# Optimization experiments

Hardware: AMD Instinct MI355X
Metric: run time of the kernel (lower is better)

## Reference

```python
import jax, jax.numpy as jnp
import numpy as np

B, S, D, H, F, NL, V = 4, 2048, 512, 8, 2048, 4, 32000
DH = D // H
EPS = 1e-6
LN_EPS = 1e-5


def _xavier(k, shape):
    lim = (6.0 / (shape[-2] + shape[-1])) ** 0.5
    return jax.random.uniform(k, shape, jnp.float32, -lim, lim)


def setup_inputs() -> dict:
    key = jax.random.key(0)
    ks = jax.random.split(key, 12)
    x = jax.random.randint(ks[0], (B, S), 0, V)
    emb = jax.random.normal(ks[1], (V, D), jnp.float32) * 0.02
    # sinusoidal positional encoding
    pos = np.arange(S, dtype=np.float32)[:, None]
    div = np.exp(np.arange(0, D, 2, dtype=np.float32) * (-np.log(10000.0) / D))
    pe_np = np.zeros((S, D), np.float32)
    pe_np[:, 0::2] = np.sin(pos * div)
    pe_np[:, 1::2] = np.cos(pos * div)
    pe = jnp.asarray(pe_np)
    return {
        "x": x, "emb": emb, "pe": pe,
        "Wq": _xavier(ks[2], (NL, D, D)), "bq": jnp.zeros((NL, D)),
        "Wk": _xavier(ks[3], (NL, D, D)), "bk": jnp.zeros((NL, D)),
        "Wv": _xavier(ks[4], (NL, D, D)), "bv": jnp.zeros((NL, D)),
        "Wo": _xavier(ks[5], (NL, D, D)), "bo": jnp.zeros((NL, D)),
        "W1": _xavier(ks[6], (NL, D, F)), "b1": jnp.zeros((NL, F)),
        "W2": _xavier(ks[7], (NL, F, D)), "b2": jnp.zeros((NL, D)),
        "g1": jnp.ones((NL, D)), "be1": jnp.zeros((NL, D)),
        "g2": jnp.ones((NL, D)), "be2": jnp.zeros((NL, D)),
        "gf": jnp.ones((D,)), "bf": jnp.zeros((D,)),
    }


def _layer_norm(h, g, b):
    mu = jnp.mean(h, axis=-1, keepdims=True)
    var = jnp.mean((h - mu) ** 2, axis=-1, keepdims=True)
    return (h - mu) * jax.lax.rsqrt(var + LN_EPS) * g + b


def _phi(u):
    # elu(x) + 1 feature map of fast-transformers causal-linear attention
    return jax.nn.elu(u) + 1.0


def _causal_linear_attention(q, k, v, key_mask):
    # q, k, v: [B, S, H, DH]; key_mask: [B, S] (1 for valid keys)
    Q = _phi(q)
    K = _phi(k) * key_mask[:, :, None, None]
    # cumulative state sum_{j<=i} K_j outer V_j : [B, S, H, DH, DH]
    St = jnp.cumsum(K[..., :, None] * v[..., None, :], axis=1)
    num = jnp.einsum("bshd,bshde->bshe", Q, St)
    Z = 1.0 / (jnp.einsum("bshd,bshd->bsh", Q, jnp.cumsum(K, axis=1)) + EPS)
    return num * Z[..., None]


def reference(x, emb, pe, Wq, bq, Wk, bk, Wv, bv, Wo, bo,
              W1, b1, W2, b2, g1, be1, g2, be2, gf, bf):
    # length mask from nonzero token count (LengthMask semantics)
    lengths = jnp.sum(jnp.abs(x) != 0, axis=-1)  # [B]
    key_mask = (jnp.arange(S)[None, :] < lengths[:, None]).astype(jnp.float32)
    h = emb[x] + pe[None, :, :]  # [B, S, D]
    for i in range(NL):
        q = (h @ Wq[i] + bq[i]).reshape(B, S, H, DH)
        k = (h @ Wk[i] + bk[i]).reshape(B, S, H, DH)
        v = (h @ Wv[i] + bv[i]).reshape(B, S, H, DH)
        a = _causal_linear_attention(q, k, v, key_mask).reshape(B, S, D)
        a = a @ Wo[i] + bo[i]
        h = _layer_norm(h + a, g1[i], be1[i])
        y = jax.nn.relu(h @ W1[i] + b1[i]) @ W2[i] + b2[i]
        h = _layer_norm(h + y, g2[i], be2[i])
    return _layer_norm(h, gf, bf)
```

## Files before the change

### kernel.cpp

```cpp
#include <hip/hip_runtime.h>
#include <math.h>

#define NLAYER 4
#define BB 4
#define SS 2048
#define DD 512
#define HH 8
#define DH 64
#define FF 2048
#define TT (BB*SS)
#define LCH 64
#define NCH (SS/LCH)
#define LN_EPS 1e-5f
#define ATT_EPS 1e-6f

typedef __bf16 bf16x8 __attribute__((ext_vector_type(8)));
typedef float  f32x4  __attribute__((ext_vector_type(4)));
typedef float  f32x16 __attribute__((ext_vector_type(16)));

__device__ __forceinline__ unsigned short f2bf(float f) {
    union { float f; unsigned u; } a; a.f = f;
    unsigned u = a.u;
    unsigned r = (u + 0x7FFFu + ((u >> 16) & 1u)) >> 16;
    return (unsigned short)r;
}
__device__ __forceinline__ float bf2f(unsigned short s) {
    union { unsigned u; float f; } a; a.u = ((unsigned)s) << 16;
    return a.f;
}
__device__ __forceinline__ float phi_f(float u) {
    return u > 0.f ? u + 1.f : __expf(u);
}

__global__ __launch_bounds__(64)
void len_kernel(const int* __restrict__ x, int* __restrict__ len) {
    const int b = blockIdx.x;
    int cnt = 0;
    for (int s = threadIdx.x; s < SS; s += 64) cnt += (x[b * SS + s] != 0);
    #pragma unroll
    for (int off = 32; off; off >>= 1) cnt += __shfl_xor(cnt, off);
    if (threadIdx.x == 0) len[b] = cnt;
}

__global__ __launch_bounds__(256)
void embed_kernel(const int* __restrict__ x, const float* __restrict__ emb,
                  const float* __restrict__ pe, unsigned short* __restrict__ h) {
    int t = blockIdx.x * 256 + threadIdx.x;
    int row = t >> 6, q = t & 63;
    int tok = x[row];
    int s = row & (SS - 1);
    const float4* ep = (const float4*)(emb + (size_t)tok * DD);
    const float4* pp = (const float4*)(pe + (size_t)s * DD);
    float4 e0 = ep[q * 2], e1 = ep[q * 2 + 1];
    float4 p0 = pp[q * 2], p1 = pp[q * 2 + 1];
    ushort4 u0 = make_ushort4(f2bf(e0.x + p0.x), f2bf(e0.y + p0.y),
                              f2bf(e0.z + p0.z), f2bf(e0.w + p0.w));
    ushort4 u1 = make_ushort4(f2bf(e1.x + p1.x), f2bf(e1.y + p1.y),
                              f2bf(e1.z + p1.z), f2bf(e1.w + p1.w));
    size_t base = (size_t)row * DD + q * 8;
    *(ushort4*)(h + base) = u0;
    *(ushort4*)(h + base + 4) = u1;
}

__global__ __launch_bounds__(256)
void transpose_cvt(const float* __restrict__ src, unsigned short* __restrict__ dst,
                   int R, int C, size_t srcLS, size_t dstLS) {
    __shared__ float tile[32][33];
    const int z = blockIdx.z;
    src += (size_t)z * srcLS;
    dst += (size_t)z * dstLS;
    const int c0 = blockIdx.x * 32, r0 = blockIdx.y * 32;
    const int tx = threadIdx.x & 31, ty = threadIdx.x >> 5;
    #pragma unroll
    for (int i = 0; i < 32; i += 8)
        tile[ty + i][tx] = src[(size_t)(r0 + ty + i) * C + c0 + tx];
    __syncthreads();
    #pragma unroll
    for (int i = 0; i < 32; i += 8)
        dst[(size_t)(c0 + ty + i) * R + r0 + tx] = f2bf(tile[tx][ty + i]);
}

__global__ __launch_bounds__(256)
void bias_concat(const float* __restrict__ bq, const float* __restrict__ bk,
                 const float* __restrict__ bv, float* __restrict__ bqkv) {
    int idx = blockIdx.x * 256 + threadIdx.x;
    if (idx >= NLAYER * 1536) return;
    int l = idx / 1536, n = idx % 1536;
    float v = n < 512 ? bq[l * 512 + n] : (n < 1024 ? bk[l * 512 + n - 512] : bv[l * 512 + n - 1024]);
    bqkv[idx] = v;
}

__device__ __forceinline__ void gll16(void* lds_ptr, const void* g_ptr) {
    __builtin_amdgcn_global_load_lds(
        (const __attribute__((address_space(1))) void*)g_ptr,
        (__attribute__((address_space(3))) void*)lds_ptr, 16, 0, 0);
}

template<int RELU, int WB>
__global__ __launch_bounds__(256, 2)
void gemm_bt(const unsigned short* __restrict__ A, const unsigned short* __restrict__ Bt,
             const float* __restrict__ bias, float* __restrict__ Cf,
             unsigned short* __restrict__ Cb, int M, int N, int K) {
    __shared__ __align__(16) char lds[2 * 2 * 128 * 64 * 2];
    const int Nt = N >> 7;
    const int bid = blockIdx.x;
    const int swz = (bid & 7) * ((int)gridDim.x >> 3) + (bid >> 3);
    const int m0 = (swz / Nt) * 128;
    const int n0 = (swz % Nt) * 128;
    const int tid = threadIdx.x;
    const int w = tid >> 6, lane = tid & 63;
    const int wr = w >> 1, wc = w & 1;
    const int srow = lane >> 3, scc = lane & 7;
    const int l32 = lane & 31, khalf = lane >> 5;

    f32x16 acc[2][2] = {};

    auto stage = [&](int buf, int k0) {
        char* base = lds + buf * 32768;
        #pragma unroll
        for (int op = 0; op < 2; ++op) {
            const unsigned short* G = op ? Bt : A;
            const int r0 = op ? n0 : m0;
            char* obase = base + op * 16384;
            #pragma unroll
            for (int i = 0; i < 4; ++i) {
                int ii = w * 4 + i;
                int row = ii * 8 + srow;
                int chunk = scc ^ (row & 7);
                gll16(obase + ii * 1024,
                      G + (size_t)(r0 + row) * K + k0 + chunk * 8);
            }
        }
    };

    stage(0, 0);
    const int nt = K >> 6;
    int buf = 0;
    const int rA = wr * 64 + l32;
    const int rB = wc * 64 + l32;

    for (int kt = 0; kt < nt; ++kt) {
        __syncthreads();
        if (kt + 1 < nt) stage(buf ^ 1, (kt + 1) << 6);
        const char* pA = lds + buf * 32768;
        const char* pB = pA + 16384;
        bf16x8 af[2][4], bfr[2][4];
        #pragma unroll
        for (int mf = 0; mf < 2; ++mf)
            #pragma unroll
            for (int kk = 0; kk < 4; ++kk) {
                int row = rA + mf * 32;
                int c = (kk * 2 + khalf) ^ (row & 7);
                af[mf][kk] = *(const bf16x8*)(pA + row * 128 + c * 16);
            }
        #pragma unroll
        for (int nf = 0; nf < 2; ++nf)
            #pragma unroll
            for (int kk = 0; kk < 4; ++kk) {
                int row = rB + nf * 32;
                int c = (kk * 2 + khalf) ^ (row & 7);
                bfr[nf][kk] = *(const bf16x8*)(pB + row * 128 + c * 16);
            }
        #pragma unroll
        for (int kk = 0; kk < 4; ++kk)
            #pragma unroll
            for (int mf = 0; mf < 2; ++mf)
                #pragma unroll
                for (int nf = 0; nf < 2; ++nf)
                    acc[mf][nf] = __builtin_amdgcn_mfma_f32_32x32x16_bf16(
                        af[mf][kk], bfr[nf][kk], acc[mf][nf], 0, 0, 0);
        buf ^= 1;
    }

    #pragma unroll
    for (int nf = 0; nf < 2; ++nf) {
        int col = n0 + wc * 64 + nf * 32 + l32;
        float bi = bias[col];
        #pragma unroll
        for (int mf = 0; mf < 2; ++mf) {
            int rowb = m0 + wr * 64 + mf * 32 + 4 * khalf;
            #pragma unroll
            for (int reg = 0; reg < 16; ++reg) {
                int row = rowb + (reg & 3) + 8 * (reg >> 2);
                float v = acc[mf][nf][reg] + bi;
                if (RELU) v = v > 0.f ? v : 0.f;
                if (WB) Cb[(size_t)row * N + col] = f2bf(v);
                else    Cf[(size_t)row * N + col] = v;
            }
        }
    }
}

__global__ __launch_bounds__(256)
void attn_chunk_sums(const unsigned short* __restrict__ qkv, const int* __restrict__ len,
                     unsigned short* __restrict__ states, float* __restrict__ ksum) {
    const int c = blockIdx.x & (NCH - 1);
    const int bh = blockIdx.x / NCH;
    const int b = bh >> 3, h = bh & 7;
    const int L = len[b];
    const int tid = threadIdx.x;
    const int w = tid >> 6, lane = tid & 63;
    __shared__ __align__(16) unsigned short Kt[64 * 64];
    __shared__ __align__(16) unsigned short Vt[64 * 64];
    __shared__ float ksumP[4][64];

    float kpart = 0.f;
    #pragma unroll 8
    for (int t = 0; t < 16; ++t) {
        const int jj = 4 * t + w;
        const int d = lane;
        const int sglob = c * 64 + jj;
        const unsigned short* base = qkv + (size_t)(b * SS + sglob) * 1536 + h * 64 + d;
        float kv = bf2f(base[512]);
        float kp = (sglob < L) ? phi_f(kv) : 0.f;
        kpart += kp;
        const int sw = (((jj >> 3) ^ (d & 7)) << 3) + (jj & 7);
        Kt[d * 64 + sw] = f2bf(kp);
        Vt[d * 64 + sw] = base[1024];
    }
    ksumP[w][lane] = kpart;
    __syncthreads();

    const int frow = w * 16 + (lane & 15);
    const int g = lane >> 4;
    bf16x8 ak[2];
    #pragma unroll
    for (int kk = 0; kk < 2; ++kk)
        ak[kk] = *(const bf16x8*)&Kt[frow * 64 + (((kk * 4 + g) ^ (frow & 7)) << 3)];
    f32x4 oc[4] = {};
    #pragma unroll
    for (int ef = 0; ef < 4; ++ef) {
        int brow = ef * 16 + (lane & 15);
        #pragma unroll
        for (int kk = 0; kk < 2; ++kk) {
            bf16x8 bv = *(const bf16x8*)&Vt[brow * 64 + (((kk * 4 + g) ^ (brow & 7)) << 3)];
            oc[ef] = __builtin_amdgcn_mfma_f32_16x16x32_bf16(ak[kk], bv, oc[ef], 0, 0, 0);
        }
    }
    unsigned short* so = states + (size_t)blockIdx.x * 4096;
    #pragma unroll
    for (int ef = 0; ef < 4; ++ef)
        #pragma unroll
        for (int r = 0; r < 4; ++r) {
            int dd = w * 16 + g * 4 + r;
            int e = ef * 16 + (lane & 15);
            so[dd * 64 + e] = f2bf(oc[ef][r]);
        }
    if (w == 0) {
        float s = ksumP[0][lane] + ksumP[1][lane] + ksumP[2][lane] + ksumP[3][lane];
        ksum[(size_t)blockIdx.x * 64 + lane] = s;
    }
}

__global__ __launch_bounds__(256)
void attn_prefix(const unsigned short* __restrict__ states, const float* __restrict__ ksum,
                 unsigned short* __restrict__ sprefix, float* __restrict__ kprefix) {
    const int bh = blockIdx.x >> 4;
    const int idx = (blockIdx.x & 15) * 256 + threadIdx.x;
    size_t base = (size_t)bh * NCH * 4096 + idx;
    float run = 0.f;
    #pragma unroll 4
    for (int cc = 0; cc < NCH; ++cc) {
        size_t o = base + (size_t)cc * 4096;
        float v = bf2f(states[o]);
        sprefix[o] = f2bf(run);
        run += v;
    }
    if ((blockIdx.x & 15) == 0 && threadIdx.x < 64) {
        size_t kb = (size_t)bh * NCH * 64 + threadIdx.x;
        float krun = 0.f;
        for (int cc = 0; cc < NCH; ++cc) {
            size_t o = kb + (size_t)cc * 64;
            float v = ksum[o];
            kprefix[o] = krun;
            krun += v;
        }
    }
}

__global__ __launch_bounds__(256)
void attn_output(const unsigned short* __restrict__ qkv, const int* __restrict__ len,
                 const unsigned short* __restrict__ sprefix, const float* __restrict__ kprefix,
                 unsigned short* __restrict__ a_bf) {
    const int c = blockIdx.x & (NCH - 1);
    const int bh = blockIdx.x / NCH;
    const int b = bh >> 3, h = bh & 7;
    const int L = len[b];
    const int tid = threadIdx.x;
    const int w = tid >> 6, lane = tid & 63;

    __shared__ __align__(16) unsigned short Qb[64 * 64];
    __shared__ __align__(16) unsigned short Kb[64 * 64];
    __shared__ __align__(16) unsigned short SpT[64 * 64];
    __shared__ __align__(16) unsigned short Vt[64 * 64];
    __shared__ __align__(16) unsigned short Amb[64 * 64];
    __shared__ float zq[64];
    __shared__ float zinv[64];

    const float kspv = kprefix[(size_t)(bh * NCH + c) * 64 + lane];
    const unsigned short* Sp = sprefix + (size_t)(bh * NCH + c) * 4096;

    #pragma unroll 4
    for (int t = 0; t < 16; ++t) {
        const int jj = 4 * t + w;
        const int d = lane;
        const int sglob = c * 64 + jj;
        const unsigned short* base = qkv + (size_t)(b * SS + sglob) * 1536 + h * 64 + d;
        float qv = bf2f(base[0]), kv = bf2f(base[512]);
        float qp = phi_f(qv);
        float kp = (sglob < L) ? phi_f(kv) : 0.f;
        const int swr = (((d >> 3) ^ (jj & 7)) << 3) + (d & 7);
        Qb[jj * 64 + swr] = f2bf(qp);
        Kb[jj * 64 + swr] = f2bf(kp);
        const int swt = (((jj >> 3) ^ (d & 7)) << 3) + (jj & 7);
        Vt[d * 64 + swt] = base[1024];
        SpT[d * 64 + swt] = Sp[jj * 64 + d];
        float zc = qp * kspv;
        #pragma unroll
        for (int off = 32; off; off >>= 1) zc += __shfl_xor(zc, off);
        if (lane == 0) zq[jj] = zc;
    }
    __syncthreads();

    const int frow = w * 16 + (lane & 15);
    const int g = lane >> 4;
    bf16x8 aq[2];
    #pragma unroll
    for (int kk = 0; kk < 2; ++kk)
        aq[kk] = *(const bf16x8*)&Qb[frow * 64 + (((kk * 4 + g) ^ (frow & 7)) << 3)];

    f32x4 am[4] = {};
    #pragma unroll
    for (int jf = 0; jf < 4; ++jf) {
        int brow = jf * 16 + (lane & 15);
        #pragma unroll
        for (int kk = 0; kk < 2; ++kk) {
            bf16x8 bk = *(const bf16x8*)&Kb[brow * 64 + (((kk * 4 + g) ^ (brow & 7)) << 3)];
            am[jf] = __builtin_amdgcn_mfma_f32_16x16x32_bf16(aq[kk], bk, am[jf], 0, 0, 0);
        }
    }

    float zl[4] = {0.f, 0.f, 0.f, 0.f};
    #pragma unroll
    for (int jf = 0; jf < 4; ++jf) {
        #pragma unroll
        for (int r = 0; r < 4; ++r) {
            int i = w * 16 + g * 4 + r;
            int j = jf * 16 + (lane & 15);
            float v = (j <= i) ? am[jf][r] : 0.f;
            zl[r] += v;
            Amb[i * 64 + (((j >> 3) ^ (i & 7)) << 3) + (j & 7)] = f2bf(v);
        }
    }
    #pragma unroll
    for (int r = 0; r < 4; ++r)
        #pragma unroll
        for (int off = 1; off < 16; off <<= 1) zl[r] += __shfl_xor(zl[r], off);
    #pragma unroll
    for (int r = 0; r < 4; ++r) {
        if ((lane & 15) == r) {
            int i = w * 16 + g * 4 + r;
            zinv[i] = 1.f / (zl[r] + zq[i] + ATT_EPS);
        }
    }

    f32x4 oc[4] = {};
    #pragma unroll
    for (int ef = 0; ef < 4; ++ef) {
        int brow = ef * 16 + (lane & 15);
        #pragma unroll
        for (int kk = 0; kk < 2; ++kk) {
            bf16x8 bs = *(const bf16x8*)&SpT[brow * 64 + (((kk * 4 + g) ^ (brow & 7)) << 3)];
            oc[ef] = __builtin_amdgcn_mfma_f32_16x16x32_bf16(aq[kk], bs, oc[ef], 0, 0, 0);
        }
    }
    bf16x8 aam[2];
    #pragma unroll
    for (int kk = 0; kk < 2; ++kk)
        aam[kk] = *(const bf16x8*)&Amb[frow * 64 + (((kk * 4 + g) ^ (frow & 7)) << 3)];
    #pragma unroll
    for (int ef = 0; ef < 4; ++ef) {
        int brow = ef * 16 + (lane & 15);
        #pragma unroll
        for (int kk = 0; kk < 2; ++kk) {
            bf16x8 bv = *(const bf16x8*)&Vt[brow * 64 + (((kk * 4 + g) ^ (brow & 7)) << 3)];
            oc[ef] = __builtin_amdgcn_mfma_f32_16x16x32_bf16(aam[kk], bv, oc[ef], 0, 0, 0);
        }
    }

    __syncthreads();
    #pragma unroll
    for (int ef = 0; ef < 4; ++ef) {
        #pragma unroll
        for (int r = 0; r < 4; ++r) {
            int i = w * 16 + g * 4 + r;
            int e = ef * 16 + (lane & 15);
            float zi = zinv[i];
            Kb[i * 64 + (((e >> 3) ^ (i & 7)) << 3) + (e & 7)] = f2bf(oc[ef][r] * zi);
        }
    }
    __syncthreads();
    {
        unsigned short* dst = a_bf + (size_t)(b * SS + c * 64) * 512 + h * 64;
        #pragma unroll
        for (int u = 0; u < 2; ++u) {
            int cid = tid + u * 256;
            int row = cid >> 3, cb = cid & 7;
            int4 val = *(const int4*)&Kb[row * 64 + ((cb ^ (row & 7)) << 3)];
            *(int4*)(dst + (size_t)row * 512 + cb * 8) = val;
        }
    }
}

template<int ADD, int FINAL>
__global__ __launch_bounds__(256)
void ln_kernel(const unsigned short* __restrict__ hin, const unsigned short* __restrict__ add,
               const float* __restrict__ gw, const float* __restrict__ bw,
               unsigned short* __restrict__ hout, float* __restrict__ fout) {
    const int row = blockIdx.x * 4 + (threadIdx.x >> 6);
    const int lane = threadIdx.x & 63;
    const size_t base = (size_t)row * DD + lane * 8;
    float v[8];
    {
        ushort4 a0 = *(const ushort4*)(hin + base);
        ushort4 a1 = *(const ushort4*)(hin + base + 4);
        v[0] = bf2f(a0.x); v[1] = bf2f(a0.y); v[2] = bf2f(a0.z); v[3] = bf2f(a0.w);
        v[4] = bf2f(a1.x); v[5] = bf2f(a1.y); v[6] = bf2f(a1.z); v[7] = bf2f(a1.w);
    }
    if (ADD) {
        ushort4 b0 = *(const ushort4*)(add + base);
        ushort4 b1 = *(const ushort4*)(add + base + 4);
        v[0] += bf2f(b0.x); v[1] += bf2f(b0.y); v[2] += bf2f(b0.z); v[3] += bf2f(b0.w);
        v[4] += bf2f(b1.x); v[5] += bf2f(b1.y); v[6] += bf2f(b1.z); v[7] += bf2f(b1.w);
    }
    float s = 0.f;
    #pragma unroll
    for (int i = 0; i < 8; ++i) s += v[i];
    #pragma unroll
    for (int off = 32; off; off >>= 1) s += __shfl_xor(s, off);
    float mu = s * (1.f / 512.f);
    float sq = 0.f;
    #pragma unroll
    for (int i = 0; i < 8; ++i) { float d = v[i] - mu; sq += d * d; }
    #pragma unroll
    for (int off = 32; off; off >>= 1) sq += __shfl_xor(sq, off);
    float rs = 1.f / sqrtf(sq * (1.f / 512.f) + LN_EPS);
    float4 g0 = ((const float4*)gw)[lane * 2], g1v = ((const float4*)gw)[lane * 2 + 1];
    float4 b0 = ((const float4*)bw)[lane * 2], b1v = ((const float4*)bw)[lane * 2 + 1];
    float gg[8] = {g0.x, g0.y, g0.z, g0.w, g1v.x, g1v.y, g1v.z, g1v.w};
    float bb[8] = {b0.x, b0.y, b0.z, b0.w, b1v.x, b1v.y, b1v.z, b1v.w};
    float o[8];
    #pragma unroll
    for (int i = 0; i < 8; ++i) o[i] = (v[i] - mu) * rs * gg[i] + bb[i];
    if (FINAL) {
        *(float4*)(fout + base)     = make_float4(o[0], o[1], o[2], o[3]);
        *(float4*)(fout + base + 4) = make_float4(o[4], o[5], o[6], o[7]);
    } else {
        *(ushort4*)(hout + base)     = make_ushort4(f2bf(o[0]), f2bf(o[1]), f2bf(o[2]), f2bf(o[3]));
        *(ushort4*)(hout + base + 4) = make_ushort4(f2bf(o[4]), f2bf(o[5]), f2bf(o[6]), f2bf(o[7]));
    }
}

extern "C" void kernel_launch(void* const* d_in, const int* in_sizes, int n_in,
                              void* d_out, int out_size, void* d_ws, size_t ws_size,
                              hipStream_t stream) {
    (void)in_sizes; (void)n_in; (void)out_size; (void)ws_size;
    const int*   x   = (const int*)d_in[0];
    const float* emb = (const float*)d_in[1];
    const float* pe  = (const float*)d_in[2];
    const float* Wq  = (const float*)d_in[3];
    const float* bq  = (const float*)d_in[4];
    const float* Wk  = (const float*)d_in[5];
    const float* bk  = (const float*)d_in[6];
    const float* Wv  = (const float*)d_in[7];
    const float* bv  = (const float*)d_in[8];
    const float* Wo  = (const float*)d_in[9];
    const float* bo  = (const float*)d_in[10];
    const float* W1  = (const float*)d_in[11];
    const float* b1  = (const float*)d_in[12];
    const float* W2  = (const float*)d_in[13];
    const float* b2  = (const float*)d_in[14];
    const float* g1  = (const float*)d_in[15];
    const float* be1 = (const float*)d_in[16];
    const float* g2  = (const float*)d_in[17];
    const float* be2 = (const float*)d_in[18];
    const float* gf  = (const float*)d_in[19];
    const float* bff = (const float*)d_in[20];
    float* out = (float*)d_out;

    char* ws = (char*)d_ws;
    size_t off = 0;
    auto alloc = [&](size_t bytes) -> void* {
        void* p = ws + off; off += (bytes + 255) & ~(size_t)255; return p;
    };
    int* len              = (int*)alloc(16);
    unsigned short* qkv_t = (unsigned short*)alloc((size_t)NLAYER * 1536 * 512 * 2);
    unsigned short* wo_t  = (unsigned short*)alloc((size_t)NLAYER * 512 * 512 * 2);
    unsigned short* w1_t  = (unsigned short*)alloc((size_t)NLAYER * 2048 * 512 * 2);
    unsigned short* w2_t  = (unsigned short*)alloc((size_t)NLAYER * 512 * 2048 * 2);
    float* bqkv           = (float*)alloc((size_t)NLAYER * 1536 * 4);
    unsigned short* h     = (unsigned short*)alloc((size_t)TT * 512 * 2);
    unsigned short* qkv   = (unsigned short*)alloc((size_t)TT * 1536 * 2);
    unsigned short* a_bf  = (unsigned short*)alloc((size_t)TT * 512 * 2);
    unsigned short* obuf  = (unsigned short*)alloc((size_t)TT * 512 * 2);
    unsigned short* y1_bf = (unsigned short*)alloc((size_t)TT * 2048 * 2);
    unsigned short* states  = (unsigned short*)alloc((size_t)32 * NCH * 4096 * 2);
    float* ksum           = (float*)alloc((size_t)32 * NCH * 64 * 4);
    unsigned short* sprefix = (unsigned short*)alloc((size_t)32 * NCH * 4096 * 2);
    float* kprefix        = (float*)alloc((size_t)32 * NCH * 64 * 4);

    len_kernel<<<BB, 64, 0, stream>>>(x, len);
    embed_kernel<<<(TT * 64) / 256, 256, 0, stream>>>(x, emb, pe, h);

    dim3 tb(256);
    transpose_cvt<<<dim3(16, 16, NLAYER), tb, 0, stream>>>(Wq, qkv_t,             512, 512, (size_t)512*512, (size_t)1536*512);
    transpose_cvt<<<dim3(16, 16, NLAYER), tb, 0, stream>>>(Wk, qkv_t + 512*512,   512, 512, (size_t)512*512, (size_t)1536*512);
    transpose_cvt<<<dim3(16, 16, NLAYER), tb, 0, stream>>>(Wv, qkv_t + 1024*512,  512, 512, (size_t)512*512, (size_t)1536*512);
    transpose_cvt<<<dim3(16, 16, NLAYER), tb, 0, stream>>>(Wo, wo_t,              512, 512, (size_t)512*512, (size_t)512*512);
    transpose_cvt<<<dim3(64, 16, NLAYER), tb, 0, stream>>>(W1, w1_t,              512, 2048, (size_t)512*2048, (size_t)2048*512);
    transpose_cvt<<<dim3(16, 64, NLAYER), tb, 0, stream>>>(W2, w2_t,              2048, 512, (size_t)2048*512, (size_t)512*2048);
    bias_concat<<<(NLAYER * 1536 + 255) / 256, 256, 0, stream>>>(bq, bk, bv, bqkv);

    for (int l = 0; l < NLAYER; ++l) {
        gemm_bt<0,1><<<(TT/128) * (1536/128), 256, 0, stream>>>(
            h, qkv_t + (size_t)l*1536*512, bqkv + l*1536, nullptr, qkv, TT, 1536, 512);
        attn_chunk_sums<<<32 * NCH, 256, 0, stream>>>(qkv, len, states, ksum);
        attn_prefix<<<32 * 16, 256, 0, stream>>>(states, ksum, sprefix, kprefix);
        attn_output<<<32 * NCH, 256, 0, stream>>>(qkv, len, sprefix, kprefix, a_bf);
        gemm_bt<0,1><<<(TT/128) * (512/128), 256, 0, stream>>>(
            a_bf, wo_t + (size_t)l*512*512, bo + l*512, nullptr, obuf, TT, 512, 512);
        ln_kernel<1,0><<<TT/4, 256, 0, stream>>>(h, obuf, g1 + l*512, be1 + l*512, h, nullptr);
        gemm_bt<1,1><<<(TT/128) * (2048/128), 256, 0, stream>>>(
            h, w1_t + (size_t)l*2048*512, b1 + l*2048, nullptr, y1_bf, TT, 2048, 512);
        gemm_bt<0,1><<<(TT/128) * (512/128), 256, 0, stream>>>(
            y1_bf, w2_t + (size_t)l*512*2048, b2 + l*512, nullptr, obuf, TT, 512, 2048);
        ln_kernel<1,0><<<TT/4, 256, 0, stream>>>(h, obuf, g2 + l*512, be2 + l*512, h, nullptr);
    }
    ln_kernel<0,1><<<TT/4, 256, 0, stream>>>(h, nullptr, gf, bff, nullptr, out);
}
```

Baseline: 552.3 us.

## Add 256x128-tile triple-buffered GEMM for QKV and FFN1 projections

Introduces gemm_big, a 512-thread GEMM with 256x128 output tiles, a three-stage LDS ring buffer with prefetch two k-tiles ahead, and a block-index swizzle. It replaces the 128x128 gemm_bt for the QKV and W1 projections. The larger tile is meant to raise operand reuse per LDS load and hide global-load latency. In exchange it uses about 144KB of LDS per block and halves the grid size, which may limit occupancy and wave balance.

```diff
diff --git a/kernel.cpp b/kernel.cpp
--- a/kernel.cpp
+++ b/kernel.cpp
@@ -186,6 +186,109 @@
                 if (RELU) v = v > 0.f ? v : 0.f;
                 if (WB) Cb[(size_t)row * N + col] = f2bf(v);
                 else    Cf[(size_t)row * N + col] = v;
+            }
+        }
+    }
+}
+
+template<int RELU>
+__global__ __launch_bounds__(512, 2)
+void gemm_big(const unsigned short* __restrict__ A, const unsigned short* __restrict__ Bt,
+              const float* __restrict__ bias, unsigned short* __restrict__ Cb,
+              int M, int N, int K) {
+    __shared__ __align__(16) char lds[3 * 49152];
+    const int Nt = N >> 7;
+    const int bid = blockIdx.x;
+    const int swz = (bid & 7) * ((int)gridDim.x >> 3) + (bid >> 3);
+    const int m0 = (swz / Nt) * 256;
+    const int n0 = (swz % Nt) * 128;
+    const int tid = threadIdx.x;
+    const int w = tid >> 6, lane = tid & 63;
+    const int wr = w >> 1, wc = w & 1;
+    const int l32 = lane & 31, khalf = lane >> 5;
+
+    f32x16 acc[2][2] = {};
+
+    auto stage = [&](int buf, int k0) {
+        char* base = lds + buf * 49152;
+        #pragma unroll
+        for (int s = 0; s < 4; ++s) {
+            int lin0 = s * 512 + w * 64;
+            int lin = lin0 + lane;
+            int row = lin >> 3, chunk = lin & 7;
+            gll16(base + lin0 * 16,
+                  A + (size_t)(m0 + row) * K + k0 + ((chunk ^ (row & 7)) << 3));
+        }
+        #pragma unroll
+        for (int s = 0; s < 2; ++s) {
+            int lin0 = s * 512 + w * 64;
+            int lin = lin0 + lane;
+            int row = lin >> 3, chunk = lin & 7;
+            gll16(base + 32768 + lin0 * 16,
+                  Bt + (size_t)(n0 + row) * K + k0 + ((chunk ^ (row & 7)) << 3));
+        }
+    };
+
+    const int nt = K >> 6;
+    stage(0, 0);
+    stage(1, 64);
+    int cur = 0;
+    const int rA = wr * 64 + l32;
+    const int rB = wc * 64 + l32;
+
+    for (int t = 0; t < nt; ++t) {
+        asm volatile("s_waitcnt lgkmcnt(0)" ::: "memory");
+        if (t + 1 < nt) asm volatile("s_waitcnt vmcnt(6)" ::: "memory");
+        else            asm volatile("s_waitcnt vmcnt(0)" ::: "memory");
+        __builtin_amdgcn_s_barrier();
+        __builtin_amdgcn_sched_barrier(0);
+        if (t + 2 < nt) {
+            int nb = cur + 2; if (nb >= 3) nb -= 3;
+            stage(nb, (t + 2) << 6);
+        }
+        const char* pA = lds + cur * 49152;
+        const char* pB = pA + 32768;
+        bf16x8 af[2][4], bfr[2][4];
+        #pragma unroll
+        for (int mf = 0; mf < 2; ++mf)
+            #pragma unroll
+            for (int kk = 0; kk < 4; ++kk) {
+                int row = rA + mf * 32;
+                int c = (kk * 2 + khalf) ^ (row & 7);
+                af[mf][kk] = *(const bf16x8*)(pA + row * 128 + c * 16);
+            }
+        #pragma unroll
+        for (int nf = 0; nf < 2; ++nf)
+            #pragma unroll
+            for (int kk = 0; kk < 4; ++kk) {
+                int row = rB + nf * 32;
+                int c = (kk * 2 + khalf) ^ (row & 7);
+                bfr[nf][kk] = *(const bf16x8*)(pB + row * 128 + c * 16);
+            }
+        #pragma unroll
+        for (int kk = 0; kk < 4; ++kk)
+            #pragma unroll
+            for (int mf = 0; mf < 2; ++mf)
+                #pragma unroll
+                for (int nf = 0; nf < 2; ++nf)
+                    acc[mf][nf] = __builtin_amdgcn_mfma_f32_32x32x16_bf16(
+                        af[mf][kk], bfr[nf][kk], acc[mf][nf], 0, 0, 0);
+        cur = (cur + 1 == 3) ? 0 : cur + 1;
+    }
+
+    #pragma unroll
+    for (int nf = 0; nf < 2; ++nf) {
+        int col = n0 + wc * 64 + nf * 32 + l32;
+        float bi = bias[col];
+        #pragma unroll
+        for (int mf = 0; mf < 2; ++mf) {
+            int rowb = m0 + wr * 64 + mf * 32 + 4 * khalf;
+            #pragma unroll
+            for (int reg = 0; reg < 16; ++reg) {
+                int row = rowb + (reg & 3) + 8 * (reg >> 2);
+                float v = acc[mf][nf][reg] + bi;
+                if (RELU) v = v > 0.f ? v : 0.f;
+                Cb[(size_t)row * N + col] = f2bf(v);
             }
         }
     }
@@ -522,16 +625,16 @@
     bias_concat<<<(NLAYER * 1536 + 255) / 256, 256, 0, stream>>>(bq, bk, bv, bqkv);
 
     for (int l = 0; l < NLAYER; ++l) {
-        gemm_bt<0,1><<<(TT/128) * (1536/128), 256, 0, stream>>>(
-            h, qkv_t + (size_t)l*1536*512, bqkv + l*1536, nullptr, qkv, TT, 1536, 512);
+        gemm_big<0><<<(TT/256) * (1536/128), 512, 0, stream>>>(
+            h, qkv_t + (size_t)l*1536*512, bqkv + l*1536, qkv, TT, 1536, 512);
         attn_chunk_sums<<<32 * NCH, 256, 0, stream>>>(qkv, len, states, ksum);
         attn_prefix<<<32 * 16, 256, 0, stream>>>(states, ksum, sprefix, kprefix);
         attn_output<<<32 * NCH, 256, 0, stream>>>(qkv, len, sprefix, kprefix, a_bf);
         gemm_bt<0,1><<<(TT/128) * (512/128), 256, 0, stream>>>(
             a_bf, wo_t + (size_t)l*512*512, bo + l*512, nullptr, obuf, TT, 512, 512);
         ln_kernel<1,0><<<TT/4, 256, 0, stream>>>(h, obuf, g1 + l*512, be1 + l*512, h, nullptr);
-        gemm_bt<1,1><<<(TT/128) * (2048/128), 256, 0, stream>>>(
-            h, w1_t + (size_t)l*2048*512, b1 + l*2048, nullptr, y1_bf, TT, 2048, 512);
+        gemm_big<1><<<(TT/256) * (2048/128), 512, 0, stream>>>(
+            h, w1_t + (size_t)l*2048*512, b1 + l*2048, y1_bf, TT, 2048, 512);
         gemm_bt<0,1><<<(TT/128) * (512/128), 256, 0, stream>>>(
             y1_bf, w2_t + (size_t)l*512*2048, b2 + l*512, nullptr, obuf, TT, 512, 2048);
         ln_kernel<1,0><<<TT/4, 256, 0, stream>>>(h, obuf, g2 + l*512, be2 + l*512, h, nullptr);
```

New measurement: 569.9 us. 1.03x slower.
